# Performance work log

Hardware: AMD Instinct MI355X
Metric: run time of the kernel (lower is better)

The kernel has to match this reference:

```python
import jax, jax.numpy as jnp
import numpy as np

N, E, V, H, HEADS, L, B = 20000, 320000, 100, 128, 3, 2, 200
NEG = 0.2   # leaky_relu negative_slope
EPS = 1e-5  # LayerNorm eps


def _mean_nodes(x, gid):
    # dgl.mean_nodes: per-graph mean of node features
    s = jax.ops.segment_sum(x, gid, num_segments=B)
    c = jax.ops.segment_sum(jnp.ones((x.shape[0], 1), x.dtype), gid, num_segments=B)
    return s / jnp.maximum(c, 1.0)


def _gat_layer(h, src, dst, Wn, bn, att, Ws, b, gamma, beta):
    # weight_node: Linear(H, H*HEADS)
    wv = (h @ Wn + bn).reshape(-1, HEADS, H)
    u = wv[src]  # [E, heads, H] gathered src features
    # attn = leaky_relu(sum(cat(u, v) * w_att)) split into u/v halves (no concat materialized)
    attn = (jnp.einsum('ehd,hd->eh', u, att[:, :H])
            + jnp.einsum('ehd,hd->eh', wv[dst], att[:, H:]))
    attn = jax.nn.leaky_relu(attn, NEG)  # [E, heads]
    # segment softmax over incoming edges of each dst node (mailbox softmax)
    m = jax.ops.segment_max(attn, dst, num_segments=N)
    m = jnp.where(jnp.isfinite(m), m, 0.0)
    e = jnp.exp(attn - m[dst])
    s = jax.ops.segment_sum(e, dst, num_segments=N)
    score = e / s[dst]
    agg = jax.ops.segment_sum(score[:, :, None] * u, dst, num_segments=N)  # [N, heads, H]
    res = agg.reshape(-1, HEADS * H) @ Ws + b
    # DGL leaves zero-in-degree nodes with zero reduced features (reduce_func never runs)
    has_in = jax.ops.segment_sum(jnp.ones((E,), h.dtype), dst, num_segments=N) > 0
    res = jnp.where(has_in[:, None], res, 0.0)
    x = res + h  # residual, then LayerNorm, relu (dropout is eval-mode identity)
    mu = jnp.mean(x, -1, keepdims=True)
    var = jnp.var(x, -1, keepdims=True)
    x = (x - mu) * jax.lax.rsqrt(var + EPS) * gamma + beta
    return jax.nn.relu(x)


def _gru_dir(x, Wih, Whh, bih, bhh, reverse):
    # torch nn.GRU single direction; x: [B, T, in]
    def step(hprev, xt):
        gi = xt @ Wih.T + bih
        gh = hprev @ Whh.T + bhh
        ir, iz, inn = jnp.split(gi, 3, -1)
        hr, hz, hn = jnp.split(gh, 3, -1)
        r = jax.nn.sigmoid(ir + hr)
        z = jax.nn.sigmoid(iz + hz)
        n = jnp.tanh(inn + r * hn)
        hnew = (1.0 - z) * n + z * hprev
        return hnew, hnew
    h0 = jnp.zeros((x.shape[0], Whh.shape[1]), x.dtype)
    hT, ys = jax.lax.scan(step, h0, jnp.swapaxes(x, 0, 1), reverse=reverse)
    return jnp.swapaxes(ys, 0, 1), hT


def setup_inputs() -> dict:
    key = jax.random.key(0)
    k = jax.random.split(key, 16)
    sc = 0.05
    return {
        'h': jax.random.normal(k[0], (N, H), jnp.float32),
        'wid': jax.random.randint(k[1], (N,), 0, V),
        'src': jax.random.randint(k[2], (E,), 0, N),
        'dst': jax.random.randint(k[3], (E,), 0, N),
        'graph_ids': jnp.sort(jax.random.randint(k[4], (N,), 0, B)),
        'proj_W': jax.random.normal(k[5], (V + H, H), jnp.float32) * sc,
        'proj_b': jnp.zeros((H,), jnp.float32),
        'conv_Wn': jax.random.normal(k[6], (L, H, HEADS * H), jnp.float32) * sc,
        'conv_bn': jnp.zeros((L, HEADS * H), jnp.float32),
        'conv_att': jax.random.normal(k[7], (L, HEADS, 2 * H), jnp.float32) * sc,
        'conv_Ws': jax.random.normal(k[8], (L, HEADS * H, H), jnp.float32) * sc,
        'conv_b': jnp.zeros((L, H), jnp.float32),
        'conv_gamma': jnp.ones((L, H), jnp.float32),
        'conv_beta': jnp.zeros((L, H), jnp.float32),
        'gru_Wih0': jax.random.normal(k[9], (2, 3 * H, H), jnp.float32) * sc,
        'gru_Whh0': jax.random.normal(k[10], (2, 3 * H, H), jnp.float32) * sc,
        'gru_bih0': jnp.zeros((2, 3 * H), jnp.float32),
        'gru_bhh0': jnp.zeros((2, 3 * H), jnp.float32),
        'gru_Wih1': jax.random.normal(k[11], (2, 3 * H, 2 * H), jnp.float32) * sc,
        'gru_Whh1': jax.random.normal(k[12], (2, 3 * H, H), jnp.float32) * sc,
        'gru_bih1': jnp.zeros((2, 3 * H), jnp.float32),
        'gru_bhh1': jnp.zeros((2, 3 * H), jnp.float32),
    }


def reference(h, wid, src, dst, graph_ids, proj_W, proj_b, conv_Wn, conv_bn, conv_att, conv_Ws, conv_b, conv_gamma, conv_beta, gru_Wih0, gru_Whh0, gru_bih0, gru_bhh0, gru_Wih1, gru_Whh1, gru_bih1, gru_bhh1):
    one_hot = jax.nn.one_hot(wid, V, dtype=h.dtype)
    hcur = jnp.concatenate([one_hot, h], -1) @ proj_W + proj_b  # project
    readouts = [_mean_nodes(hcur, graph_ids)]
    for l in range(L):
        hcur = _gat_layer(hcur, src, dst, conv_Wn[l], conv_bn[l], conv_att[l],
                          conv_Ws[l], conv_b[l], conv_gamma[l], conv_beta[l])
        readouts.append(_mean_nodes(hcur, graph_ids))
    x = jnp.stack(readouts, 1)  # [B, L+1, H] GRU readout sequence
    finals = []
    for (Wih, Whh, bih, bhh) in ((gru_Wih0, gru_Whh0, gru_bih0, gru_bhh0),
                                 (gru_Wih1, gru_Whh1, gru_bih1, gru_bhh1)):
        yf, hf = _gru_dir(x, Wih[0], Whh[0], bih[0], bhh[0], False)
        yb, hb = _gru_dir(x, Wih[1], Whh[1], bih[1], bhh[1], True)
        x = jnp.concatenate([yf, yb], -1)
        finals += [hf, hb]
    # torch returns h_n [num_layers*2, B, H]; module takes mean over dim 0
    return jnp.mean(jnp.stack(finals, 0), 0)  # [B, H]
```

## Files before the change

### kernel.cpp

```cpp
#include <hip/hip_runtime.h>
#include <cstddef>
#include <cstdint>

static constexpr int Nn    = 20000;
static constexpr int Ee    = 320000;
static constexpr int Vv    = 100;
static constexpr int Hh    = 128;
static constexpr int HEADS = 3;
static constexpr int Bb    = 200;
static constexpr float NEG = 0.2f;
static constexpr float EPS = 1e-5f;

typedef short bf16x8 __attribute__((ext_vector_type(8)));
typedef float f32x4  __attribute__((ext_vector_type(4)));

__device__ inline unsigned short bf16_rne(float x) {
    unsigned u = __builtin_bit_cast(unsigned, x);
    u += 0x7FFFu + ((u >> 16) & 1u);
    return (unsigned short)(u >> 16);
}
__device__ inline float bf16_f(unsigned short h) {
    unsigned u = ((unsigned)h) << 16;
    return __builtin_bit_cast(float, u);
}
__device__ inline float bf_lo(unsigned u) { return __builtin_bit_cast(float, u << 16); }
__device__ inline float bf_hi(unsigned u) { return __builtin_bit_cast(float, u & 0xFFFF0000u); }
__device__ inline float lrelu(float a) { return a >= 0.f ? a : NEG * a; }
__device__ inline float sigmoidf(float x) { return 1.f / (1.f + __expf(-x)); }

__global__ __launch_bounds__(1024) void scan_offsets(const int* __restrict__ deg,
                                                     int* __restrict__ offs,
                                                     int* __restrict__ cur) {
    __shared__ int sums[1024];
    const int tid = threadIdx.x;
    const int per = (Nn + 1023) >> 10;
    int begin = tid * per;
    int end = begin + per; if (end > Nn) end = Nn;
    if (begin > Nn) begin = Nn;
    int s = 0;
    for (int i = begin; i < end; i++) s += deg[i];
    sums[tid] = s;
    __syncthreads();
    for (int off = 1; off < 1024; off <<= 1) {
        int v = (tid >= off) ? sums[tid - off] : 0;
        __syncthreads();
        sums[tid] += v;
        __syncthreads();
    }
    int run = sums[tid] - s;
    for (int i = begin; i < end; i++) {
        offs[i] = run; cur[i] = run;
        run += deg[i];
    }
    if (end == Nn) offs[Nn] = run;
}

__global__ void fill_csr(const int* __restrict__ dst, const int* __restrict__ src,
                         int* __restrict__ cur, int* __restrict__ csrc) {
    for (int i = blockIdx.x * blockDim.x + threadIdx.x; i < Ee; i += gridDim.x * blockDim.x) {
        int p = atomicAdd(&cur[dst[i]], 1);
        csrc[p] = src[i];
    }
}

struct PrepArgs {
    const float *projW, *convWn, *convWs, *convAtt, *convBn, *convB;
    const float *Wih0, *Whh0, *Wih1, *Whh1;
    const int *gid, *dst;
    unsigned short *pBth, *pBtl;
    unsigned short *WfTh0, *WfTl0, *WfTh1, *WfTl1;
    float *vavd, *vc, *biasF;
    float *WihT0, *WhhT0, *WihT1, *WhhT1;
    int *goffs, *deg;
};

__device__ inline void wsplit(const float* B, int K, int N, int idx,
                              unsigned short* Bth, unsigned short* Btl) {
    int k = idx / N, n = idx - k * N;
    float v = B[idx];
    unsigned short h = bf16_rne(v);
    unsigned short l = bf16_rne(v - bf16_f(h));
    Bth[(size_t)n * K + k] = h;
    Btl[(size_t)n * K + k] = l;
}
__device__ inline void gruT(const float* W, int K, int idx, float* WT) {
    int d = idx / (384 * K);
    int r = idx - d * 384 * K;
    int j = r / K, k = r - j * K;
    WT[(size_t)d * K * 384 + (size_t)k * 384 + j] = W[idx];
}

__global__ void prep_all(PrepArgs a) {
    int i = blockIdx.x * blockDim.x + threadIdx.x;
    if (i < 16384) { wsplit(a.projW, 128, 128, i, a.pBth, a.pBtl); return; } i -= 16384;
#pragma unroll
    for (int l = 0; l < 2; l++) {
        if (i < 49152) {
            int k = i >> 7, c = i & 127;
            int h = k >> 7, i_ = k & 127;
            const float* wn = a.convWn + (size_t)l * 49152 + (size_t)i_ * 384 + h * 128;
            const float* ws = a.convWs + (size_t)l * 49152 + (size_t)(h * 128) * 128 + c;
            float v = 0.f;
            for (int j = 0; j < 128; j++) v += wn[j] * ws[(size_t)j * 128];
            unsigned short hi = bf16_rne(v);
            unsigned short lo = bf16_rne(v - bf16_f(hi));
            unsigned short* th = l ? a.WfTh1 : a.WfTh0;
            unsigned short* tl = l ? a.WfTl1 : a.WfTl0;
            th[(size_t)c * 384 + k] = hi;
            tl[(size_t)c * 384 + k] = lo;
            return;
        }
        i -= 49152;
    }
    if (i < 1536) {
        int l = i / 768, r = i % 768;
        int sd = r / 384, rr = r % 384, h = rr >> 7, i_ = rr & 127;
        const float* wn = a.convWn + (size_t)l * 49152 + (size_t)i_ * 384 + h * 128;
        const float* at = a.convAtt + l * 768 + h * 256 + sd * 128;
        float v = 0.f;
        for (int j = 0; j < 128; j++) v += wn[j] * at[j];
        a.vavd[i] = v;
        return;
    } i -= 1536;
    if (i < 12) {
        int l = i / 6, r = i % 6, sd = r / 3, h = r % 3;
        const float* bn = a.convBn + l * 384 + h * 128;
        const float* at = a.convAtt + l * 768 + h * 256 + sd * 128;
        float v = 0.f;
        for (int j = 0; j < 128; j++) v += bn[j] * at[j];
        a.vc[i] = v;
        return;
    } i -= 12;
    if (i < 256) {
        int l = i >> 7, c = i & 127;
        const float* bn = a.convBn + l * 384;
        const float* ws = a.convWs + (size_t)l * 49152 + c;
        float v = a.convB[l * 128 + c];
        for (int k = 0; k < 384; k++) v += bn[k] * ws[(size_t)k * 128];
        a.biasF[i] = v;
        return;
    } i -= 256;
    if (i < 98304)  { gruT(a.Wih0, 128, i, a.WihT0); return; }  i -= 98304;
    if (i < 98304)  { gruT(a.Whh0, 128, i, a.WhhT0); return; }  i -= 98304;
    if (i < 196608) { gruT(a.Wih1, 256, i, a.WihT1); return; }  i -= 196608;
    if (i < 98304)  { gruT(a.Whh1, 128, i, a.WhhT1); return; }  i -= 98304;
    if (i < Nn) {
        int g = a.gid[i];
        if (i == 0) { for (int b = 0; b <= g; b++) a.goffs[b] = 0; }
        else { int pg = a.gid[i - 1]; for (int b = pg + 1; b <= g; b++) a.goffs[b] = i; }
        if (i == Nn - 1) { for (int b = g + 1; b <= Bb; b++) a.goffs[b] = Nn; }
        return;
    } i -= Nn;
    if (i < Ee) atomicAdd(&a.deg[a.dst[i]], 1);
}

struct GArgs {
    const float* A; const unsigned short* Bth; const unsigned short* Btl;
    const float* bias; int M, K;
    const int* wid; const float* projW;
    const int* deg; const float* gamma; const float* beta;
    float* hcur;
    const int* gid; float* reado;
    const float* vavd; const float* vc;
    float* adf; float* addf;
    unsigned short* hb;
};

template <int MODE>
__global__ __launch_bounds__(256) void gemm_fused(GArgs a) {
    __shared__ unsigned short As_hi[32][40];
    __shared__ unsigned short As_lo[32][40];
    __shared__ unsigned short Bs_hi[128][40];
    __shared__ unsigned short Bs_lo[128][40];
    __shared__ float ytile[32][132];
    __shared__ float sred[6][32][4];
    __shared__ int sgid[32];
    const int tid  = threadIdx.x;
    const int row0 = blockIdx.y * 32;
    const int wn   = tid >> 6;
    const int L    = tid & 63;
    const int lrow = L & 15;
    const int lq   = L >> 4;
    const int K = a.K;

    f32x4 acc[2][2];
#pragma unroll
    for (int i = 0; i < 2; i++)
#pragma unroll
        for (int j = 0; j < 2; j++) acc[i][j] = (f32x4){0.f, 0.f, 0.f, 0.f};

    for (int kb = 0; kb < K; kb += 32) {
        {
            int m  = tid >> 3;
            int kq = (tid & 7) * 4;
            float4 v = *(const float4*)(a.A + (size_t)(row0 + m) * K + kb + kq);
            unsigned short h0 = bf16_rne(v.x), h1 = bf16_rne(v.y),
                           h2 = bf16_rne(v.z), h3 = bf16_rne(v.w);
            *(short4*)&As_hi[m][kq] = make_short4((short)h0, (short)h1, (short)h2, (short)h3);
            *(short4*)&As_lo[m][kq] = make_short4((short)bf16_rne(v.x - bf16_f(h0)),
                                                  (short)bf16_rne(v.y - bf16_f(h1)),
                                                  (short)bf16_rne(v.z - bf16_f(h2)),
                                                  (short)bf16_rne(v.w - bf16_f(h3)));
        }
        {
            int n  = tid >> 1;
            int kh = (tid & 1) * 16;
            const unsigned short* sh = a.Bth + (size_t)n * K + kb + kh;
            const unsigned short* sl = a.Btl + (size_t)n * K + kb + kh;
            *(float4*)&Bs_hi[n][kh]     = *(const float4*)sh;
            *(float4*)&Bs_hi[n][kh + 8] = *(const float4*)(sh + 8);
            *(float4*)&Bs_lo[n][kh]     = *(const float4*)sl;
            *(float4*)&Bs_lo[n][kh + 8] = *(const float4*)(sl + 8);
        }
        __syncthreads();
        bf16x8 ah[2], al[2], bh[2], bl[2];
#pragma unroll
        for (int mi = 0; mi < 2; mi++) {
            int r = mi * 16 + lrow;
            ah[mi] = *(const bf16x8*)&As_hi[r][lq * 8];
            al[mi] = *(const bf16x8*)&As_lo[r][lq * 8];
        }
#pragma unroll
        for (int ni = 0; ni < 2; ni++) {
            int r = wn * 32 + ni * 16 + lrow;
            bh[ni] = *(const bf16x8*)&Bs_hi[r][lq * 8];
            bl[ni] = *(const bf16x8*)&Bs_lo[r][lq * 8];
        }
#pragma unroll
        for (int mi = 0; mi < 2; mi++)
#pragma unroll
            for (int ni = 0; ni < 2; ni++) {
                acc[mi][ni] = __builtin_amdgcn_mfma_f32_16x16x32_bf16(ah[mi], bh[ni], acc[mi][ni], 0, 0, 0);
                acc[mi][ni] = __builtin_amdgcn_mfma_f32_16x16x32_bf16(ah[mi], bl[ni], acc[mi][ni], 0, 0, 0);
                acc[mi][ni] = __builtin_amdgcn_mfma_f32_16x16x32_bf16(al[mi], bh[ni], acc[mi][ni], 0, 0, 0);
            }
        __syncthreads();
    }

#pragma unroll
    for (int ni = 0; ni < 2; ni++) {
        float bb = a.bias[wn * 32 + ni * 16 + lrow];
#pragma unroll
        for (int mi = 0; mi < 2; mi++)
#pragma unroll
            for (int r = 0; r < 4; r++) acc[mi][ni][r] += bb;
    }

    if constexpr (MODE == 0) {
#pragma unroll
        for (int mi = 0; mi < 2; mi++)
#pragma unroll
            for (int r = 0; r < 4; r++) {
                int lr = mi * 16 + lq * 4 + r;
                int row = row0 + lr;
                int wi = a.wid[row];
#pragma unroll
                for (int ni = 0; ni < 2; ni++) {
                    int c = wn * 32 + ni * 16 + lrow;
                    float y = acc[mi][ni][r] + a.projW[(size_t)wi * 128 + c];
                    acc[mi][ni][r] = y;
                    a.hcur[(size_t)row * 128 + c] = y;
                    ytile[lr][c] = y;
                }
            }
    }

    if constexpr (MODE == 2) {
        __shared__ float red1[32][4], red2[32][4];
        float g4[2], be4[2];
#pragma unroll
        for (int ni = 0; ni < 2; ni++) {
            int c = wn * 32 + ni * 16 + lrow;
            g4[ni] = a.gamma[c]; be4[ni] = a.beta[c];
        }
#pragma unroll
        for (int mi = 0; mi < 2; mi++)
#pragma unroll
            for (int r = 0; r < 4; r++) {
                int lr = mi * 16 + lq * 4 + r;
                int row = row0 + lr;
                int dg = a.deg[row];
#pragma unroll
                for (int ni = 0; ni < 2; ni++) {
                    int c = wn * 32 + ni * 16 + lrow;
                    float hold = a.hcur[(size_t)row * 128 + c];
                    acc[mi][ni][r] = hold + (dg > 0 ? acc[mi][ni][r] : 0.f);
                }
            }
#pragma unroll
        for (int mi = 0; mi < 2; mi++)
#pragma unroll
            for (int r = 0; r < 4; r++) {
                float ps = acc[mi][0][r] + acc[mi][1][r];
#pragma unroll
                for (int o = 1; o < 16; o <<= 1) ps += __shfl_xor(ps, o, 64);
                if (lrow == 0) red1[mi * 16 + lq * 4 + r][wn] = ps;
            }
        __syncthreads();
#pragma unroll
        for (int mi = 0; mi < 2; mi++)
#pragma unroll
            for (int r = 0; r < 4; r++) {
                int lr = mi * 16 + lq * 4 + r;
                float mu = (red1[lr][0] + red1[lr][1] + red1[lr][2] + red1[lr][3]) * (1.f / 128.f);
                float qs = 0.f;
#pragma unroll
                for (int ni = 0; ni < 2; ni++) {
                    float dx = acc[mi][ni][r] - mu;
                    qs += dx * dx;
                }
#pragma unroll
                for (int o = 1; o < 16; o <<= 1) qs += __shfl_xor(qs, o, 64);
                if (lrow == 0) red2[lr][wn] = qs;
            }
        __syncthreads();
#pragma unroll
        for (int mi = 0; mi < 2; mi++)
#pragma unroll
            for (int r = 0; r < 4; r++) {
                int lr = mi * 16 + lq * 4 + r;
                int row = row0 + lr;
                float mu = (red1[lr][0] + red1[lr][1] + red1[lr][2] + red1[lr][3]) * (1.f / 128.f);
                float var = (red2[lr][0] + red2[lr][1] + red2[lr][2] + red2[lr][3]) * (1.f / 128.f);
                float rs = rsqrtf(var + EPS);
#pragma unroll
                for (int ni = 0; ni < 2; ni++) {
                    int c = wn * 32 + ni * 16 + lrow;
                    float y = fmaxf((acc[mi][ni][r] - mu) * rs * g4[ni] + be4[ni], 0.f);
                    acc[mi][ni][r] = y;
                    a.hcur[(size_t)row * 128 + c] = y;
                    ytile[lr][c] = y;
                }
            }
    }

    if (tid < 32) sgid[tid] = a.gid[row0 + tid];

    const bool dots = (a.vavd != nullptr);
    if (dots) {
        float vv0[6], vv1[6];
#pragma unroll
        for (int d = 0; d < 6; d++) {
            vv0[d] = a.vavd[d * 128 + wn * 32 + lrow];
            vv1[d] = a.vavd[d * 128 + wn * 32 + 16 + lrow];
        }
#pragma unroll
        for (int d = 0; d < 6; d++) {
#pragma unroll
            for (int mi = 0; mi < 2; mi++)
#pragma unroll
                for (int r = 0; r < 4; r++) {
                    float ps = acc[mi][0][r] * vv0[d] + acc[mi][1][r] * vv1[d];
#pragma unroll
                    for (int o = 1; o < 16; o <<= 1) ps += __shfl_xor(ps, o, 64);
                    if (lrow == 0) sred[d][mi * 16 + lq * 4 + r][wn] = ps;
                }
        }
    }
    __syncthreads();

    {
        int j = tid & 127, hh = tid >> 7;
        float sum = 0.f; int curg = -1;
        for (int r = hh * 16; r < hh * 16 + 16; r++) {
            int g = sgid[r];
            if (g != curg) {
                if (curg >= 0) atomicAdd(&a.reado[(size_t)curg * 128 + j], sum);
                sum = 0.f; curg = g;
            }
            sum += ytile[r][j];
        }
        if (curg >= 0) atomicAdd(&a.reado[(size_t)curg * 128 + j], sum);
    }

    if (dots) {
        if (tid < 192) {
            int row = tid & 31, d = tid >> 5;
            float s = sred[d][row][0] + sred[d][row][1] + sred[d][row][2] + sred[d][row][3]
                    + a.vc[d];
            int node = row0 + row;
            int sd = d / 3, h = d - sd * 3;
            float* dstp = sd ? a.addf : a.adf;
            dstp[(size_t)node * 4 + h] = s;
        }
        {
            int row = tid >> 3, c0 = (tid & 7) * 16;
            unsigned* dst = (unsigned*)(a.hb + (size_t)(row0 + row) * 128 + c0);
#pragma unroll
            for (int q = 0; q < 8; q++) {
                unsigned lo = bf16_rne(ytile[row][c0 + 2 * q]);
                unsigned hi = bf16_rne(ytile[row][c0 + 2 * q + 1]);
                dst[q] = lo | (hi << 16);
            }
        }
    }
}

__global__ __launch_bounds__(256) void gat_gather(const unsigned short* __restrict__ hb,
                                                  const float4* __restrict__ ad,
                                                  const float4* __restrict__ add,
                                                  const int* __restrict__ offs,
                                                  const int* __restrict__ csrc,
                                                  float* __restrict__ T) {
    __shared__ float4 slot[4][64];
    const int n = (blockIdx.x * 256 + threadIdx.x) >> 6;
    const int wv_ = threadIdx.x >> 6;
    const int L = threadIdx.x & 63;
    if (n >= Nn) return;
    const int start = offs[n];
    const int deg = offs[n + 1] - start;
    float2* o2 = (float2*)(T + (size_t)n * 384);
    if (deg == 0) {
        float2 z = make_float2(0.f, 0.f);
        o2[L] = z; o2[64 + L] = z; o2[128 + L] = z;
        return;
    }
    const float4 adn = add[n];
    float2 t0 = make_float2(0.f, 0.f), t1 = t0, t2 = t0;

    if (deg <= 64) {
        int sn = 0; float e0 = 0.f, e1 = 0.f, e2 = 0.f;
        if (L < deg) {
            sn = csrc[start + L];
            float4 a4 = ad[sn];
            e0 = __expf(lrelu(a4.x + adn.x));
            e1 = __expf(lrelu(a4.y + adn.y));
            e2 = __expf(lrelu(a4.z + adn.z));
        }
        float s0 = e0, s1 = e1, s2 = e2;
#pragma unroll
        for (int o = 32; o > 0; o >>= 1) {
            s0 += __shfl_xor(s0, o, 64);
            s1 += __shfl_xor(s1, o, 64);
            s2 += __shfl_xor(s2, o, 64);
        }
        slot[wv_][L] = make_float4(__builtin_bit_cast(float, sn),
                                   e0 / s0, e1 / s1, e2 / s2);
        __builtin_amdgcn_wave_barrier();
#pragma unroll 2
        for (int j = 0; j < deg; j++) {
            float4 sc = slot[wv_][j];
            int s_n = __builtin_bit_cast(int, sc.x);
            unsigned u = ((const unsigned*)(hb + (size_t)s_n * 128))[L];
            float x0 = bf_lo(u), x1 = bf_hi(u);
            t0.x += sc.y * x0; t0.y += sc.y * x1;
            t1.x += sc.z * x0; t1.y += sc.z * x1;
            t2.x += sc.w * x0; t2.y += sc.w * x1;
        }
    } else {
        float s0 = 0.f, s1 = 0.f, s2 = 0.f;
        for (int i = L; i < deg; i += 64) {
            int sn = csrc[start + i];
            float4 a4 = ad[sn];
            s0 += __expf(lrelu(a4.x + adn.x));
            s1 += __expf(lrelu(a4.y + adn.y));
            s2 += __expf(lrelu(a4.z + adn.z));
        }
#pragma unroll
        for (int o = 32; o > 0; o >>= 1) {
            s0 += __shfl_xor(s0, o, 64);
            s1 += __shfl_xor(s1, o, 64);
            s2 += __shfl_xor(s2, o, 64);
        }
        float i0 = 1.f / s0, i1 = 1.f / s1, i2 = 1.f / s2;
        for (int base = 0; base < deg; base += 64) {
            int cnt = deg - base; if (cnt > 64) cnt = 64;
            if (L < cnt) {
                int sn = csrc[start + base + L];
                float4 a4 = ad[sn];
                slot[wv_][L] = make_float4(__builtin_bit_cast(float, sn),
                                           __expf(lrelu(a4.x + adn.x)) * i0,
                                           __expf(lrelu(a4.y + adn.y)) * i1,
                                           __expf(lrelu(a4.z + adn.z)) * i2);
            }
            __builtin_amdgcn_wave_barrier();
            for (int j = 0; j < cnt; j++) {
                float4 sc = slot[wv_][j];
                int s_n = __builtin_bit_cast(int, sc.x);
                unsigned u = ((const unsigned*)(hb + (size_t)s_n * 128))[L];
                float x0 = bf_lo(u), x1 = bf_hi(u);
                t0.x += sc.y * x0; t0.y += sc.y * x1;
                t1.x += sc.z * x0; t1.y += sc.z * x1;
                t2.x += sc.w * x0; t2.y += sc.w * x1;
            }
            __builtin_amdgcn_wave_barrier();
        }
    }
    o2[L] = t0; o2[64 + L] = t1; o2[128 + L] = t2;
}

__global__ __launch_bounds__(768) void gru_all(const float* __restrict__ reado,
                                               const int* __restrict__ goffs,
                                               const float* __restrict__ WihT0,
                                               const float* __restrict__ WhhT0,
                                               const float* __restrict__ bih0,
                                               const float* __restrict__ bhh0,
                                               const float* __restrict__ WihT1,
                                               const float* __restrict__ WhhT1,
                                               const float* __restrict__ bih1,
                                               const float* __restrict__ bhh1,
                                               float* __restrict__ out) {
    const int b = blockIdx.x;
    const int tid = threadIdx.x;
    const int dir = tid / 384;
    const int j = tid - dir * 384;
    __shared__ float xs[3][128];
    __shared__ float y0s[3][256];
    __shared__ float hs[2][128];
    __shared__ float gil[2][384], ghl[2][384];
    __shared__ float fin01[2][128];
    if (tid < 128) {
        int cnt = goffs[b + 1] - goffs[b];
        float invc = 1.f / fmaxf((float)cnt, 1.f);
#pragma unroll
        for (int t = 0; t < 3; t++)
            xs[t][tid] = reado[(size_t)t * Bb * Hh + (size_t)b * Hh + tid] * invc;
    }
    if (j < 128) hs[dir][j] = 0.f;
    __syncthreads();
    {
        const float* Wi = WihT0 + (size_t)dir * 128 * 384;
        const float* Wh = WhhT0 + (size_t)dir * 128 * 384;
        float gi[3];
        gi[0] = gi[1] = gi[2] = bih0[dir * 384 + j];
        for (int k = 0; k < 128; k++) {
            float w = Wi[(size_t)k * 384 + j];
            gi[0] += w * xs[0][k]; gi[1] += w * xs[1][k]; gi[2] += w * xs[2][k];
        }
        const float bhj = bhh0[dir * 384 + j];
        for (int step = 0; step < 3; step++) {
            int t = dir ? 2 - step : step;
            float g = bhj;
            for (int k = 0; k < 128; k++) g += Wh[(size_t)k * 384 + j] * hs[dir][k];
            ghl[dir][j] = g;
            gil[dir][j] = gi[t];
            __syncthreads();
            if (j < 128) {
                float r = sigmoidf(gil[dir][j] + ghl[dir][j]);
                float z = sigmoidf(gil[dir][j + 128] + ghl[dir][j + 128]);
                float nn2 = tanhf(gil[dir][j + 256] + r * ghl[dir][j + 256]);
                float hnew = (1.f - z) * nn2 + z * hs[dir][j];
                hs[dir][j] = hnew;
                y0s[t][dir * 128 + j] = hnew;
                if (step == 2) fin01[dir][j] = hnew;
            }
            __syncthreads();
        }
    }
    if (j < 128) hs[dir][j] = 0.f;
    {
        const float* Wi = WihT1 + (size_t)dir * 256 * 384;
        const float* Wh = WhhT1 + (size_t)dir * 128 * 384;
        float gi[3];
        gi[0] = gi[1] = gi[2] = bih1[dir * 384 + j];
        for (int k = 0; k < 256; k++) {
            float w = Wi[(size_t)k * 384 + j];
            gi[0] += w * y0s[0][k]; gi[1] += w * y0s[1][k]; gi[2] += w * y0s[2][k];
        }
        const float bhj = bhh1[dir * 384 + j];
        __syncthreads();
        for (int step = 0; step < 3; step++) {
            int t = dir ? 2 - step : step;
            float g = bhj;
            for (int k = 0; k < 128; k++) g += Wh[(size_t)k * 384 + j] * hs[dir][k];
            ghl[dir][j] = g;
            gil[dir][j] = gi[t];
            __syncthreads();
            if (j < 128) {
                float r = sigmoidf(gil[dir][j] + ghl[dir][j]);
                float z = sigmoidf(gil[dir][j + 128] + ghl[dir][j + 128]);
                float nn2 = tanhf(gil[dir][j + 256] + r * ghl[dir][j + 256]);
                float hnew = (1.f - z) * nn2 + z * hs[dir][j];
                hs[dir][j] = hnew;
                if (step == 2) xs[dir][j] = hnew;
            }
            __syncthreads();
        }
    }
    if (tid < 128)
        out[(size_t)b * Hh + tid] = 0.25f * (fin01[0][tid] + fin01[1][tid] +
                                             xs[0][tid] + xs[1][tid]);
}

extern "C" void kernel_launch(void* const* d_in, const int* in_sizes, int n_in,
                              void* d_out, int out_size, void* d_ws, size_t ws_size,
                              hipStream_t stream) {
    const float* h      = (const float*)d_in[0];
    const int*   wid    = (const int*)d_in[1];
    const int*   src    = (const int*)d_in[2];
    const int*   dst    = (const int*)d_in[3];
    const int*   gid    = (const int*)d_in[4];
    const float* projW  = (const float*)d_in[5];
    const float* projB  = (const float*)d_in[6];
    const float* convWn = (const float*)d_in[7];
    const float* convBn = (const float*)d_in[8];
    const float* convAtt= (const float*)d_in[9];
    const float* convWs = (const float*)d_in[10];
    const float* convB  = (const float*)d_in[11];
    const float* convG  = (const float*)d_in[12];
    const float* convBe = (const float*)d_in[13];
    const float* Wih0   = (const float*)d_in[14];
    const float* Whh0   = (const float*)d_in[15];
    const float* bih0   = (const float*)d_in[16];
    const float* bhh0   = (const float*)d_in[17];
    const float* Wih1   = (const float*)d_in[18];
    const float* Whh1   = (const float*)d_in[19];
    const float* bih1   = (const float*)d_in[20];
    const float* bhh1   = (const float*)d_in[21];
    float* out = (float*)d_out;

    char* p = (char*)d_ws;
    auto align16 = [&]() { p = (char*)(((uintptr_t)p + 15) & ~(uintptr_t)15); };
    auto alloc_f = [&](size_t n) { align16(); float* r = (float*)p; p += n * sizeof(float); return r; };
    auto alloc_i = [&](size_t n) { align16(); int* r = (int*)p; p += n * sizeof(int); return r; };
    auto alloc_s = [&](size_t n) { align16(); unsigned short* r = (unsigned short*)p; p += n * sizeof(unsigned short); return r; };
    float* hcur  = alloc_f((size_t)Nn * 128);
    float* T     = alloc_f((size_t)Nn * 384);
    float* adbuf = alloc_f((size_t)Nn * 4);
    float* addbuf= alloc_f((size_t)Nn * 4);
    float* reado = alloc_f((size_t)3 * Bb * Hh);
    int* deg  = alloc_i(Nn);
    const size_t zero_bytes = (size_t)3 * Bb * Hh * sizeof(float) + Nn * sizeof(int);
    float* WihT0 = alloc_f((size_t)2 * 128 * 384);
    float* WhhT0 = alloc_f((size_t)2 * 128 * 384);
    float* WihT1 = alloc_f((size_t)2 * 256 * 384);
    float* WhhT1 = alloc_f((size_t)2 * 128 * 384);
    float* vavd  = alloc_f(1536);
    float* vc    = alloc_f(12);
    float* biasF = alloc_f(256);
    int* offs = alloc_i(Nn + 1);
    int* cur  = alloc_i(Nn);
    int* csrc = alloc_i(Ee);
    int* goffs = alloc_i(Bb + 1);
    unsigned short* hb = alloc_s((size_t)Nn * 128);
    unsigned short* pBth = alloc_s(128 * 128);
    unsigned short* pBtl = alloc_s(128 * 128);
    unsigned short* WfTh[2] = { alloc_s(128 * 384), alloc_s(128 * 384) };
    unsigned short* WfTl[2] = { alloc_s(128 * 384), alloc_s(128 * 384) };

    hipMemsetAsync(reado, 0, zero_bytes, stream);

    PrepArgs pa;
    pa.projW = projW + (size_t)Vv * Hh;
    pa.convWn = convWn; pa.convWs = convWs; pa.convAtt = convAtt;
    pa.convBn = convBn; pa.convB = convB;
    pa.Wih0 = Wih0; pa.Whh0 = Whh0; pa.Wih1 = Wih1; pa.Whh1 = Whh1;
    pa.gid = gid; pa.dst = dst;
    pa.pBth = pBth; pa.pBtl = pBtl;
    pa.WfTh0 = WfTh[0]; pa.WfTl0 = WfTl[0]; pa.WfTh1 = WfTh[1]; pa.WfTl1 = WfTl[1];
    pa.vavd = vavd; pa.vc = vc; pa.biasF = biasF;
    pa.WihT0 = WihT0; pa.WhhT0 = WhhT0; pa.WihT1 = WihT1; pa.WhhT1 = WhhT1;
    pa.goffs = goffs; pa.deg = deg;
    const int prep_total = 16384 + 2 * 49152 + 1536 + 12 + 256 + 98304 + 98304 + 196608 + 98304 + Nn + Ee;
    prep_all<<<(prep_total + 255) / 256, 256, 0, stream>>>(pa);

    scan_offsets<<<1, 1024, 0, stream>>>(deg, offs, cur);
    fill_csr<<<1250, 256, 0, stream>>>(dst, src, cur, csrc);

    {
        GArgs g = {};
        g.A = h; g.Bth = pBth; g.Btl = pBtl; g.bias = projB;
        g.M = Nn; g.K = 128;
        g.wid = wid; g.projW = projW; g.hcur = hcur;
        g.gid = gid; g.reado = reado;
        g.vavd = vavd; g.vc = vc; g.adf = adbuf; g.addf = addbuf; g.hb = hb;
        gemm_fused<0><<<dim3(1, Nn / 32), 256, 0, stream>>>(g);
    }

    const int nwaveblocks = (Nn * 64 + 255) / 256;
    for (int l = 0; l < 2; l++) {
        gat_gather<<<nwaveblocks, 256, 0, stream>>>(hb, (const float4*)adbuf, (const float4*)addbuf,
                                                    offs, csrc, T);
        {
            GArgs g = {};
            g.A = T; g.Bth = WfTh[l]; g.Btl = WfTl[l]; g.bias = biasF + l * 128;
            g.M = Nn; g.K = 384;
            g.deg = deg; g.gamma = convG + l * Hh; g.beta = convBe + l * Hh;
            g.hcur = hcur;
            g.gid = gid; g.reado = reado + (size_t)(l + 1) * Bb * Hh;
            if (l == 0) { g.vavd = vavd + 768; g.vc = vc + 6; g.adf = adbuf; g.addf = addbuf; g.hb = hb; }
            gemm_fused<2><<<dim3(1, Nn / 32), 256, 0, stream>>>(g);
        }
    }

    gru_all<<<Bb, 768, 0, stream>>>(reado, goffs, WihT0, WhhT0, bih0, bhh0,
                                    WihT1, WhhT1, bih1, bhh1, out);
}
```

Baseline: 368.2 us.

## Split GRU into per-layer kernels batching two graphs with register-cached weights

Replaces the single per-graph GRU kernel with two kernels, one per GRU layer, each launched over (graph pair, direction). Each block handles two graphs so every weight load serves two sequences, and the recurrent weights are held in a 128-entry register array across the three timesteps. The layer-0 output goes through a global buffer, and final states are summed into the output with atomics after a memset. This aims to cut the redundant weight traffic and the long serial per-block chain of the old kernel, at the cost of an extra launch, heavy register pressure, and float atomics that make the summation order nondeterministic.

```diff
diff --git a/kernel.cpp b/kernel.cpp
--- a/kernel.cpp
+++ b/kernel.cpp
@@ -489,97 +489,176 @@
     o2[L] = t0; o2[64 + L] = t1; o2[128 + L] = t2;
 }
 
-__global__ __launch_bounds__(768) void gru_all(const float* __restrict__ reado,
-                                               const int* __restrict__ goffs,
-                                               const float* __restrict__ WihT0,
-                                               const float* __restrict__ WhhT0,
-                                               const float* __restrict__ bih0,
-                                               const float* __restrict__ bhh0,
-                                               const float* __restrict__ WihT1,
-                                               const float* __restrict__ WhhT1,
-                                               const float* __restrict__ bih1,
-                                               const float* __restrict__ bhh1,
-                                               float* __restrict__ out) {
-    const int b = blockIdx.x;
-    const int tid = threadIdx.x;
-    const int dir = tid / 384;
-    const int j = tid - dir * 384;
-    __shared__ float xs[3][128];
-    __shared__ float y0s[3][256];
-    __shared__ float hs[2][128];
-    __shared__ float gil[2][384], ghl[2][384];
-    __shared__ float fin01[2][128];
-    if (tid < 128) {
-        int cnt = goffs[b + 1] - goffs[b];
-        float invc = 1.f / fmaxf((float)cnt, 1.f);
-#pragma unroll
-        for (int t = 0; t < 3; t++)
-            xs[t][tid] = reado[(size_t)t * Bb * Hh + (size_t)b * Hh + tid] * invc;
-    }
-    if (j < 128) hs[dir][j] = 0.f;
+static constexpr int GNB = 2;
+
+__global__ __launch_bounds__(384, 2) void gru_l0(const float* __restrict__ reado,
+                                                 const int* __restrict__ goffs,
+                                                 const float* __restrict__ WihT0,
+                                                 const float* __restrict__ WhhT0,
+                                                 const float* __restrict__ bih0,
+                                                 const float* __restrict__ bhh0,
+                                                 float* __restrict__ y0g,
+                                                 float* __restrict__ out) {
+    const int dir = blockIdx.y;
+    const int b0 = blockIdx.x * GNB;
+    const int j = threadIdx.x;
+    __shared__ float xs[3][128][GNB];
+    __shared__ float hs[128][GNB];
+    __shared__ float gis[384][GNB];
+    __shared__ float ghs[384][GNB];
+    __shared__ float invc_s[GNB];
+    if (j < GNB) {
+        int cnt = goffs[b0 + j + 1] - goffs[b0 + j];
+        invc_s[j] = 1.f / fmaxf((float)cnt, 1.f);
+    }
+    if (j < 128) {
+#pragma unroll
+        for (int nb = 0; nb < GNB; nb++) hs[j][nb] = 0.f;
+    }
     __syncthreads();
-    {
-        const float* Wi = WihT0 + (size_t)dir * 128 * 384;
-        const float* Wh = WhhT0 + (size_t)dir * 128 * 384;
-        float gi[3];
-        gi[0] = gi[1] = gi[2] = bih0[dir * 384 + j];
+    for (int i = j; i < 3 * 128 * GNB; i += 384) {
+        int nb = i % GNB, k = (i / GNB) & 127, t = i / (128 * GNB);
+        xs[t][k][nb] = reado[(size_t)t * Bb * Hh + (size_t)(b0 + nb) * Hh + k] * invc_s[nb];
+    }
+    __syncthreads();
+
+    const float* Wi = WihT0 + (size_t)dir * 128 * 384;
+    const float* Wh = WhhT0 + (size_t)dir * 128 * 384;
+    const float bij = bih0[dir * 384 + j];
+    const float bhj = bhh0[dir * 384 + j];
+    int tmap[3];
+    tmap[0] = dir ? 2 : 0; tmap[1] = 1; tmap[2] = dir ? 0 : 2;
+
+    float gi[3][GNB];
+#pragma unroll
+    for (int s = 0; s < 3; s++)
+#pragma unroll
+        for (int nb = 0; nb < GNB; nb++) gi[s][nb] = bij;
+    for (int k = 0; k < 128; k++) {
+        float w = Wi[(size_t)k * 384 + j];
+#pragma unroll
+        for (int s = 0; s < 3; s++)
+#pragma unroll
+            for (int nb = 0; nb < GNB; nb++)
+                gi[s][nb] += w * xs[tmap[s]][k][nb];
+    }
+
+    float wh[128];
+#pragma unroll
+    for (int k = 0; k < 128; k++) wh[k] = Wh[(size_t)k * 384 + j];
+
+#pragma unroll
+    for (int step = 0; step < 3; step++) {
+        float g[GNB];
+#pragma unroll
+        for (int nb = 0; nb < GNB; nb++) g[nb] = bhj;
+#pragma unroll
         for (int k = 0; k < 128; k++) {
-            float w = Wi[(size_t)k * 384 + j];
-            gi[0] += w * xs[0][k]; gi[1] += w * xs[1][k]; gi[2] += w * xs[2][k];
-        }
-        const float bhj = bhh0[dir * 384 + j];
-        for (int step = 0; step < 3; step++) {
-            int t = dir ? 2 - step : step;
-            float g = bhj;
-            for (int k = 0; k < 128; k++) g += Wh[(size_t)k * 384 + j] * hs[dir][k];
-            ghl[dir][j] = g;
-            gil[dir][j] = gi[t];
-            __syncthreads();
-            if (j < 128) {
-                float r = sigmoidf(gil[dir][j] + ghl[dir][j]);
-                float z = sigmoidf(gil[dir][j + 128] + ghl[dir][j + 128]);
-                float nn2 = tanhf(gil[dir][j + 256] + r * ghl[dir][j + 256]);
-                float hnew = (1.f - z) * nn2 + z * hs[dir][j];
-                hs[dir][j] = hnew;
-                y0s[t][dir * 128 + j] = hnew;
-                if (step == 2) fin01[dir][j] = hnew;
-            }
-            __syncthreads();
-        }
-    }
-    if (j < 128) hs[dir][j] = 0.f;
-    {
-        const float* Wi = WihT1 + (size_t)dir * 256 * 384;
-        const float* Wh = WhhT1 + (size_t)dir * 128 * 384;
-        float gi[3];
-        gi[0] = gi[1] = gi[2] = bih1[dir * 384 + j];
-        for (int k = 0; k < 256; k++) {
-            float w = Wi[(size_t)k * 384 + j];
-            gi[0] += w * y0s[0][k]; gi[1] += w * y0s[1][k]; gi[2] += w * y0s[2][k];
-        }
-        const float bhj = bhh1[dir * 384 + j];
-        __syncthreads();
-        for (int step = 0; step < 3; step++) {
-            int t = dir ? 2 - step : step;
-            float g = bhj;
-            for (int k = 0; k < 128; k++) g += Wh[(size_t)k * 384 + j] * hs[dir][k];
-            ghl[dir][j] = g;
-            gil[dir][j] = gi[t];
-            __syncthreads();
-            if (j < 128) {
-                float r = sigmoidf(gil[dir][j] + ghl[dir][j]);
-                float z = sigmoidf(gil[dir][j + 128] + ghl[dir][j + 128]);
-                float nn2 = tanhf(gil[dir][j + 256] + r * ghl[dir][j + 256]);
-                float hnew = (1.f - z) * nn2 + z * hs[dir][j];
-                hs[dir][j] = hnew;
-                if (step == 2) xs[dir][j] = hnew;
-            }
-            __syncthreads();
-        }
-    }
-    if (tid < 128)
-        out[(size_t)b * Hh + tid] = 0.25f * (fin01[0][tid] + fin01[1][tid] +
-                                             xs[0][tid] + xs[1][tid]);
+#pragma unroll
+            for (int nb = 0; nb < GNB; nb++) g[nb] += wh[k] * hs[k][nb];
+        }
+#pragma unroll
+        for (int nb = 0; nb < GNB; nb++) {
+            ghs[j][nb] = g[nb];
+            gis[j][nb] = gi[step][nb];
+        }
+        __syncthreads();
+        if (j < 128) {
+            const int t = tmap[step];
+#pragma unroll
+            for (int nb = 0; nb < GNB; nb++) {
+                float r  = sigmoidf(gis[j][nb] + ghs[j][nb]);
+                float z  = sigmoidf(gis[j + 128][nb] + ghs[j + 128][nb]);
+                float nn = tanhf(gis[j + 256][nb] + r * ghs[j + 256][nb]);
+                float hnew = (1.f - z) * nn + z * hs[j][nb];
+                hs[j][nb] = hnew;
+                y0g[((size_t)t * Bb + (b0 + nb)) * 256 + dir * 128 + j] = hnew;
+                if (step == 2)
+                    atomicAdd(&out[(size_t)(b0 + nb) * Hh + j], 0.25f * hnew);
+            }
+        }
+        __syncthreads();
+    }
+}
+
+__global__ __launch_bounds__(384, 2) void gru_l1(const float* __restrict__ y0g,
+                                                 const float* __restrict__ WihT1,
+                                                 const float* __restrict__ WhhT1,
+                                                 const float* __restrict__ bih1,
+                                                 const float* __restrict__ bhh1,
+                                                 float* __restrict__ out) {
+    const int dir = blockIdx.y;
+    const int b0 = blockIdx.x * GNB;
+    const int j = threadIdx.x;
+    __shared__ float ys[3][256][GNB];
+    __shared__ float hs[128][GNB];
+    __shared__ float gis[384][GNB];
+    __shared__ float ghs[384][GNB];
+    if (j < 128) {
+#pragma unroll
+        for (int nb = 0; nb < GNB; nb++) hs[j][nb] = 0.f;
+    }
+    for (int i = j; i < 3 * 256 * GNB; i += 384) {
+        int nb = i % GNB, u = (i / GNB) & 255, t = i / (256 * GNB);
+        ys[t][u][nb] = y0g[((size_t)t * Bb + (b0 + nb)) * 256 + u];
+    }
+    __syncthreads();
+
+    const float* Wi = WihT1 + (size_t)dir * 256 * 384;
+    const float* Wh = WhhT1 + (size_t)dir * 128 * 384;
+    const float bij = bih1[dir * 384 + j];
+    const float bhj = bhh1[dir * 384 + j];
+    int tmap[3];
+    tmap[0] = dir ? 2 : 0; tmap[1] = 1; tmap[2] = dir ? 0 : 2;
+
+    float gi[3][GNB];
+#pragma unroll
+    for (int s = 0; s < 3; s++)
+#pragma unroll
+        for (int nb = 0; nb < GNB; nb++) gi[s][nb] = bij;
+    for (int k = 0; k < 256; k++) {
+        float w = Wi[(size_t)k * 384 + j];
+#pragma unroll
+        for (int s = 0; s < 3; s++)
+#pragma unroll
+            for (int nb = 0; nb < GNB; nb++)
+                gi[s][nb] += w * ys[tmap[s]][k][nb];
+    }
+
+    float wh[128];
+#pragma unroll
+    for (int k = 0; k < 128; k++) wh[k] = Wh[(size_t)k * 384 + j];
+
+#pragma unroll
+    for (int step = 0; step < 3; step++) {
+        float g[GNB];
+#pragma unroll
+        for (int nb = 0; nb < GNB; nb++) g[nb] = bhj;
+#pragma unroll
+        for (int k = 0; k < 128; k++) {
+#pragma unroll
+            for (int nb = 0; nb < GNB; nb++) g[nb] += wh[k] * hs[k][nb];
+        }
+#pragma unroll
+        for (int nb = 0; nb < GNB; nb++) {
+            ghs[j][nb] = g[nb];
+            gis[j][nb] = gi[step][nb];
+        }
+        __syncthreads();
+        if (j < 128) {
+#pragma unroll
+            for (int nb = 0; nb < GNB; nb++) {
+                float r  = sigmoidf(gis[j][nb] + ghs[j][nb]);
+                float z  = sigmoidf(gis[j + 128][nb] + ghs[j + 128][nb]);
+                float nn = tanhf(gis[j + 256][nb] + r * ghs[j + 256][nb]);
+                float hnew = (1.f - z) * nn + z * hs[j][nb];
+                hs[j][nb] = hnew;
+                if (step == 2)
+                    atomicAdd(&out[(size_t)(b0 + nb) * Hh + j], 0.25f * hnew);
+            }
+        }
+        __syncthreads();
+    }
 }
 
 extern "C" void kernel_launch(void* const* d_in, const int* in_sizes, int n_in,
@@ -628,6 +707,7 @@
     float* vavd  = alloc_f(1536);
     float* vc    = alloc_f(12);
     float* biasF = alloc_f(256);
+    float* y0g   = alloc_f((size_t)3 * Bb * 256);
     int* offs = alloc_i(Nn + 1);
     int* cur  = alloc_i(Nn);
     int* csrc = alloc_i(Ee);
@@ -639,6 +719,7 @@
     unsigned short* WfTl[2] = { alloc_s(128 * 384), alloc_s(128 * 384) };
 
     hipMemsetAsync(reado, 0, zero_bytes, stream);
+    hipMemsetAsync(out, 0, (size_t)Bb * Hh * sizeof(float), stream);
 
     PrepArgs pa;
     pa.projW = projW + (size_t)Vv * Hh;
@@ -683,6 +764,7 @@
         }
     }
 
-    gru_all<<<Bb, 768, 0, stream>>>(reado, goffs, WihT0, WhhT0, bih0, bhh0,
-                                    WihT1, WhhT1, bih1, bhh1, out);
-}
+    gru_l0<<<dim3(Bb / GNB, 2), 384, 0, stream>>>(reado, goffs, WihT0, WhhT0, bih0, bhh0,
+                                                  y0g, out);
+    gru_l1<<<dim3(Bb / GNB, 2), 384, 0, stream>>>(y0g, WihT1, WhhT1, bih1, bhh1, out);
+}
```

After: 397.5 us. 1.08x slower.

## Split GRU into per-direction layer kernels and drop weight transposes in prep

Applied to the files above, without the earlier changes.

The single GRU kernel, one 768-thread block per graph, becomes two kernels, one per layer, each launched with a block per (graph, direction). The weights are now read in their original row-major layout with float4 loads per thread, so the transposes of about 500K GRU weight elements in prep_all are removed. The first recurrent matvec is skipped because the hidden state starts at zero. Final states are accumulated into out with atomicAdd after a memset. This adds a kernel launch and a global round trip for the layer-0 outputs, and the per-thread row reads are strided across threads, so they coalesce less well than the old transposed reads.

```diff
diff --git a/kernel.cpp b/kernel.cpp
--- a/kernel.cpp
+++ b/kernel.cpp
@@ -65,12 +65,10 @@
 
 struct PrepArgs {
     const float *projW, *convWn, *convWs, *convAtt, *convBn, *convB;
-    const float *Wih0, *Whh0, *Wih1, *Whh1;
     const int *gid, *dst;
     unsigned short *pBth, *pBtl;
     unsigned short *WfTh0, *WfTl0, *WfTh1, *WfTl1;
     float *vavd, *vc, *biasF;
-    float *WihT0, *WhhT0, *WihT1, *WhhT1;
     int *goffs, *deg;
 };
 
@@ -82,12 +80,6 @@
     unsigned short l = bf16_rne(v - bf16_f(h));
     Bth[(size_t)n * K + k] = h;
     Btl[(size_t)n * K + k] = l;
-}
-__device__ inline void gruT(const float* W, int K, int idx, float* WT) {
-    int d = idx / (384 * K);
-    int r = idx - d * 384 * K;
-    int j = r / K, k = r - j * K;
-    WT[(size_t)d * K * 384 + (size_t)k * 384 + j] = W[idx];
 }
 
 __global__ void prep_all(PrepArgs a) {
@@ -140,10 +132,6 @@
         a.biasF[i] = v;
         return;
     } i -= 256;
-    if (i < 98304)  { gruT(a.Wih0, 128, i, a.WihT0); return; }  i -= 98304;
-    if (i < 98304)  { gruT(a.Whh0, 128, i, a.WhhT0); return; }  i -= 98304;
-    if (i < 196608) { gruT(a.Wih1, 256, i, a.WihT1); return; }  i -= 196608;
-    if (i < 98304)  { gruT(a.Whh1, 128, i, a.WhhT1); return; }  i -= 98304;
     if (i < Nn) {
         int g = a.gid[i];
         if (i == 0) { for (int b = 0; b <= g; b++) a.goffs[b] = 0; }
@@ -489,97 +477,139 @@
     o2[L] = t0; o2[64 + L] = t1; o2[128 + L] = t2;
 }
 
-__global__ __launch_bounds__(768) void gru_all(const float* __restrict__ reado,
-                                               const int* __restrict__ goffs,
-                                               const float* __restrict__ WihT0,
-                                               const float* __restrict__ WhhT0,
-                                               const float* __restrict__ bih0,
-                                               const float* __restrict__ bhh0,
-                                               const float* __restrict__ WihT1,
-                                               const float* __restrict__ WhhT1,
-                                               const float* __restrict__ bih1,
-                                               const float* __restrict__ bhh1,
-                                               float* __restrict__ out) {
+__global__ __launch_bounds__(384) void gru_l0(const float* __restrict__ reado,
+                                              const int* __restrict__ goffs,
+                                              const float* __restrict__ Wih,
+                                              const float* __restrict__ Whh,
+                                              const float* __restrict__ bih,
+                                              const float* __restrict__ bhh,
+                                              float* __restrict__ y0g,
+                                              float* __restrict__ out) {
+    const int dir = blockIdx.y;
     const int b = blockIdx.x;
-    const int tid = threadIdx.x;
-    const int dir = tid / 384;
-    const int j = tid - dir * 384;
+    const int j = threadIdx.x;
     __shared__ float xs[3][128];
-    __shared__ float y0s[3][256];
-    __shared__ float hs[2][128];
-    __shared__ float gil[2][384], ghl[2][384];
-    __shared__ float fin01[2][128];
-    if (tid < 128) {
-        int cnt = goffs[b + 1] - goffs[b];
-        float invc = 1.f / fmaxf((float)cnt, 1.f);
-#pragma unroll
-        for (int t = 0; t < 3; t++)
-            xs[t][tid] = reado[(size_t)t * Bb * Hh + (size_t)b * Hh + tid] * invc;
-    }
-    if (j < 128) hs[dir][j] = 0.f;
+    __shared__ float hs[128];
+    __shared__ float gil[384], ghl[384];
+
+    const float invc = 1.f / fmaxf((float)(goffs[b + 1] - goffs[b]), 1.f);
+    {
+        int t = j >> 7, k = j & 127;
+        xs[t][k] = reado[(size_t)t * Bb * Hh + (size_t)b * Hh + k] * invc;
+    }
+    if (j < 128) hs[j] = 0.f;
     __syncthreads();
-    {
-        const float* Wi = WihT0 + (size_t)dir * 128 * 384;
-        const float* Wh = WhhT0 + (size_t)dir * 128 * 384;
-        float gi[3];
-        gi[0] = gi[1] = gi[2] = bih0[dir * 384 + j];
-        for (int k = 0; k < 128; k++) {
-            float w = Wi[(size_t)k * 384 + j];
-            gi[0] += w * xs[0][k]; gi[1] += w * xs[1][k]; gi[2] += w * xs[2][k];
-        }
-        const float bhj = bhh0[dir * 384 + j];
-        for (int step = 0; step < 3; step++) {
-            int t = dir ? 2 - step : step;
-            float g = bhj;
-            for (int k = 0; k < 128; k++) g += Wh[(size_t)k * 384 + j] * hs[dir][k];
-            ghl[dir][j] = g;
-            gil[dir][j] = gi[t];
-            __syncthreads();
-            if (j < 128) {
-                float r = sigmoidf(gil[dir][j] + ghl[dir][j]);
-                float z = sigmoidf(gil[dir][j + 128] + ghl[dir][j + 128]);
-                float nn2 = tanhf(gil[dir][j + 256] + r * ghl[dir][j + 256]);
-                float hnew = (1.f - z) * nn2 + z * hs[dir][j];
-                hs[dir][j] = hnew;
-                y0s[t][dir * 128 + j] = hnew;
-                if (step == 2) fin01[dir][j] = hnew;
-            }
-            __syncthreads();
-        }
-    }
-    if (j < 128) hs[dir][j] = 0.f;
-    {
-        const float* Wi = WihT1 + (size_t)dir * 256 * 384;
-        const float* Wh = WhhT1 + (size_t)dir * 128 * 384;
-        float gi[3];
-        gi[0] = gi[1] = gi[2] = bih1[dir * 384 + j];
-        for (int k = 0; k < 256; k++) {
-            float w = Wi[(size_t)k * 384 + j];
-            gi[0] += w * y0s[0][k]; gi[1] += w * y0s[1][k]; gi[2] += w * y0s[2][k];
-        }
-        const float bhj = bhh1[dir * 384 + j];
-        __syncthreads();
-        for (int step = 0; step < 3; step++) {
-            int t = dir ? 2 - step : step;
-            float g = bhj;
-            for (int k = 0; k < 128; k++) g += Wh[(size_t)k * 384 + j] * hs[dir][k];
-            ghl[dir][j] = g;
-            gil[dir][j] = gi[t];
-            __syncthreads();
-            if (j < 128) {
-                float r = sigmoidf(gil[dir][j] + ghl[dir][j]);
-                float z = sigmoidf(gil[dir][j + 128] + ghl[dir][j + 128]);
-                float nn2 = tanhf(gil[dir][j + 256] + r * ghl[dir][j + 256]);
-                float hnew = (1.f - z) * nn2 + z * hs[dir][j];
-                hs[dir][j] = hnew;
-                if (step == 2) xs[dir][j] = hnew;
-            }
-            __syncthreads();
-        }
-    }
-    if (tid < 128)
-        out[(size_t)b * Hh + tid] = 0.25f * (fin01[0][tid] + fin01[1][tid] +
-                                             xs[0][tid] + xs[1][tid]);
+
+    const float* Wi = Wih + ((size_t)dir * 384 + j) * 128;
+    const float* Wh = Whh + ((size_t)dir * 384 + j) * 128;
+    const float bij = bih[dir * 384 + j];
+    const float bhj = bhh[dir * 384 + j];
+
+    float gi0 = bij, gi1 = bij, gi2 = bij;
+#pragma unroll 4
+    for (int k = 0; k < 128; k += 4) {
+        float4 w  = *(const float4*)(Wi + k);
+        float4 x0 = *(const float4*)&xs[0][k];
+        float4 x1 = *(const float4*)&xs[1][k];
+        float4 x2 = *(const float4*)&xs[2][k];
+        gi0 += w.x * x0.x + w.y * x0.y + w.z * x0.z + w.w * x0.w;
+        gi1 += w.x * x1.x + w.y * x1.y + w.z * x1.z + w.w * x1.w;
+        gi2 += w.x * x2.x + w.y * x2.y + w.z * x2.z + w.w * x2.w;
+    }
+
+#pragma unroll
+    for (int step = 0; step < 3; step++) {
+        float g = bhj;
+        if (step > 0) {
+#pragma unroll 4
+            for (int k = 0; k < 128; k += 4) {
+                float4 w  = *(const float4*)(Wh + k);
+                float4 hv = *(const float4*)&hs[k];
+                g += w.x * hv.x + w.y * hv.y + w.z * hv.z + w.w * hv.w;
+            }
+        }
+        ghl[j] = g;
+        gil[j] = dir ? (step == 0 ? gi2 : (step == 1 ? gi1 : gi0))
+                     : (step == 0 ? gi0 : (step == 1 ? gi1 : gi2));
+        __syncthreads();
+        if (j < 128) {
+            const int t = dir ? 2 - step : step;
+            float r  = sigmoidf(gil[j] + ghl[j]);
+            float z  = sigmoidf(gil[j + 128] + ghl[j + 128]);
+            float nn = tanhf(gil[j + 256] + r * ghl[j + 256]);
+            float hnew = (1.f - z) * nn + z * hs[j];
+            hs[j] = hnew;
+            y0g[((size_t)t * Bb + b) * 256 + dir * 128 + j] = hnew;
+            if (step == 2)
+                atomicAdd(&out[(size_t)b * Hh + j], 0.25f * hnew);
+        }
+        __syncthreads();
+    }
+}
+
+__global__ __launch_bounds__(384) void gru_l1(const float* __restrict__ y0g,
+                                              const float* __restrict__ Wih,
+                                              const float* __restrict__ Whh,
+                                              const float* __restrict__ bih,
+                                              const float* __restrict__ bhh,
+                                              float* __restrict__ out) {
+    const int dir = blockIdx.y;
+    const int b = blockIdx.x;
+    const int j = threadIdx.x;
+    __shared__ float ys[3][256];
+    __shared__ float hs[128];
+    __shared__ float gil[384], ghl[384];
+
+    for (int i = j; i < 3 * 256; i += 384) {
+        int t = i >> 8, u = i & 255;
+        ys[t][u] = y0g[((size_t)t * Bb + b) * 256 + u];
+    }
+    if (j < 128) hs[j] = 0.f;
+    __syncthreads();
+
+    const float* Wi = Wih + ((size_t)dir * 384 + j) * 256;
+    const float* Wh = Whh + ((size_t)dir * 384 + j) * 128;
+    const float bij = bih[dir * 384 + j];
+    const float bhj = bhh[dir * 384 + j];
+
+    float gi0 = bij, gi1 = bij, gi2 = bij;
+#pragma unroll 4
+    for (int k = 0; k < 256; k += 4) {
+        float4 w  = *(const float4*)(Wi + k);
+        float4 x0 = *(const float4*)&ys[0][k];
+        float4 x1 = *(const float4*)&ys[1][k];
+        float4 x2 = *(const float4*)&ys[2][k];
+        gi0 += w.x * x0.x + w.y * x0.y + w.z * x0.z + w.w * x0.w;
+        gi1 += w.x * x1.x + w.y * x1.y + w.z * x1.z + w.w * x1.w;
+        gi2 += w.x * x2.x + w.y * x2.y + w.z * x2.z + w.w * x2.w;
+    }
+
+#pragma unroll
+    for (int step = 0; step < 3; step++) {
+        float g = bhj;
+        if (step > 0) {
+#pragma unroll 4
+            for (int k = 0; k < 128; k += 4) {
+                float4 w  = *(const float4*)(Wh + k);
+                float4 hv = *(const float4*)&hs[k];
+                g += w.x * hv.x + w.y * hv.y + w.z * hv.z + w.w * hv.w;
+            }
+        }
+        ghl[j] = g;
+        gil[j] = dir ? (step == 0 ? gi2 : (step == 1 ? gi1 : gi0))
+                     : (step == 0 ? gi0 : (step == 1 ? gi1 : gi2));
+        __syncthreads();
+        if (j < 128) {
+            float r  = sigmoidf(gil[j] + ghl[j]);
+            float z  = sigmoidf(gil[j + 128] + ghl[j + 128]);
+            float nn = tanhf(gil[j + 256] + r * ghl[j + 256]);
+            float hnew = (1.f - z) * nn + z * hs[j];
+            hs[j] = hnew;
+            if (step == 2)
+                atomicAdd(&out[(size_t)b * Hh + j], 0.25f * hnew);
+        }
+        __syncthreads();
+    }
 }
 
 extern "C" void kernel_launch(void* const* d_in, const int* in_sizes, int n_in,
@@ -621,13 +651,10 @@
     float* reado = alloc_f((size_t)3 * Bb * Hh);
     int* deg  = alloc_i(Nn);
     const size_t zero_bytes = (size_t)3 * Bb * Hh * sizeof(float) + Nn * sizeof(int);
-    float* WihT0 = alloc_f((size_t)2 * 128 * 384);
-    float* WhhT0 = alloc_f((size_t)2 * 128 * 384);
-    float* WihT1 = alloc_f((size_t)2 * 256 * 384);
-    float* WhhT1 = alloc_f((size_t)2 * 128 * 384);
     float* vavd  = alloc_f(1536);
     float* vc    = alloc_f(12);
     float* biasF = alloc_f(256);
+    float* y0g   = alloc_f((size_t)3 * Bb * 256);
     int* offs = alloc_i(Nn + 1);
     int* cur  = alloc_i(Nn);
     int* csrc = alloc_i(Ee);
@@ -639,19 +666,18 @@
     unsigned short* WfTl[2] = { alloc_s(128 * 384), alloc_s(128 * 384) };
 
     hipMemsetAsync(reado, 0, zero_bytes, stream);
+    hipMemsetAsync(out, 0, (size_t)Bb * Hh * sizeof(float), stream);
 
     PrepArgs pa;
     pa.projW = projW + (size_t)Vv * Hh;
     pa.convWn = convWn; pa.convWs = convWs; pa.convAtt = convAtt;
     pa.convBn = convBn; pa.convB = convB;
-    pa.Wih0 = Wih0; pa.Whh0 = Whh0; pa.Wih1 = Wih1; pa.Whh1 = Whh1;
     pa.gid = gid; pa.dst = dst;
     pa.pBth = pBth; pa.pBtl = pBtl;
     pa.WfTh0 = WfTh[0]; pa.WfTl0 = WfTl[0]; pa.WfTh1 = WfTh[1]; pa.WfTl1 = WfTl[1];
     pa.vavd = vavd; pa.vc = vc; pa.biasF = biasF;
-    pa.WihT0 = WihT0; pa.WhhT0 = WhhT0; pa.WihT1 = WihT1; pa.WhhT1 = WhhT1;
     pa.goffs = goffs; pa.deg = deg;
-    const int prep_total = 16384 + 2 * 49152 + 1536 + 12 + 256 + 98304 + 98304 + 196608 + 98304 + Nn + Ee;
+    const int prep_total = 16384 + 2 * 49152 + 1536 + 12 + 256 + Nn + Ee;
     prep_all<<<(prep_total + 255) / 256, 256, 0, stream>>>(pa);
 
     scan_offsets<<<1, 1024, 0, stream>>>(deg, offs, cur);
@@ -683,6 +709,7 @@
         }
     }
 
-    gru_all<<<Bb, 768, 0, stream>>>(reado, goffs, WihT0, WhhT0, bih0, bhh0,
-                                    WihT1, WhhT1, bih1, bhh1, out);
-}
+    gru_l0<<<dim3(Bb, 2), 384, 0, stream>>>(reado, goffs, Wih0, Whh0, bih0, bhh0,
+                                            y0g, out);
+    gru_l1<<<dim3(Bb, 2), 384, 0, stream>>>(y0g, Wih1, Whh1, bih1, bhh1, out);
+}
```

After: 408.2 us. 10.9% more time.
